# Optimization experiments

Measured on AMD Instinct MI355X. Metric: run time of the kernel, lower is better.

The kernel has to match this reference:

```python
import jax, jax.numpy as jnp
import numpy as np

B, N, M = 4, 512, 8192
QUERY_DIM, INPUT_DIM = 512, 256
HEADS, DIM_HEAD = 8, 64
ATT_DIM = HEADS * DIM_HEAD  # 512


def setup_inputs() -> dict:
    key = jax.random.key(0)
    ks = jax.random.split(key, 6)
    x = jax.random.normal(ks[0], (B, N, QUERY_DIM), dtype=jnp.float32)
    context = jax.random.normal(ks[1], (B, M, INPUT_DIM), dtype=jnp.float32)
    # Linear weights stored as [in, out] for x @ W
    Wq = jax.random.normal(ks[2], (QUERY_DIM, ATT_DIM), dtype=jnp.float32) / np.sqrt(QUERY_DIM)
    Wkv = jax.random.normal(ks[3], (INPUT_DIM, 2 * ATT_DIM), dtype=jnp.float32) / np.sqrt(INPUT_DIM)
    Wo = jax.random.normal(ks[4], (ATT_DIM, QUERY_DIM), dtype=jnp.float32) / np.sqrt(ATT_DIM)
    bo = jax.random.normal(ks[5], (QUERY_DIM,), dtype=jnp.float32) * 0.01
    return {"x": x, "context": context, "Wq": Wq, "Wkv": Wkv, "Wo": Wo, "bo": bo}


def reference(x, context, Wq, Wkv, Wo, bo):
    scale = DIM_HEAD ** -0.5
    q = x @ Wq                      # [B, N, H*D]
    kv = context @ Wkv              # [B, M, 2*H*D]
    k, v = jnp.split(kv, 2, axis=-1)
    # split heads: b n (h d) -> b h n d
    q = q.reshape(B, N, HEADS, DIM_HEAD).transpose(0, 2, 1, 3)
    k = k.reshape(B, M, HEADS, DIM_HEAD).transpose(0, 2, 1, 3)
    v = v.reshape(B, M, HEADS, DIM_HEAD).transpose(0, 2, 1, 3)
    scores = jnp.einsum('bhid,bhjd->bhij', q, k) * scale  # [B, H, N, M]
    attn = jax.nn.softmax(scores, axis=-1)
    out = jnp.einsum('bhij,bhjd->bhid', attn, v)           # [B, H, N, D]
    out = out.transpose(0, 2, 1, 3).reshape(B, N, ATT_DIM)
    return out @ Wo + bo
```

## Files before the change

kernel.cpp:

```cpp
#include <hip/hip_runtime.h>
#include <hip/hip_bf16.h>
#include <cstdint>

#define NB 4
#define NQ 512
#define NM 8192
#define NH 8
#define DH 64

typedef short bf16x8s __attribute__((ext_vector_type(8)));
typedef short bf16x4s __attribute__((ext_vector_type(4)));
typedef float f32x4  __attribute__((ext_vector_type(4)));

static __device__ __forceinline__ short f2bs(float f) {
    unsigned u = __builtin_bit_cast(unsigned, f);
    return (short)(unsigned short)((u + 0x8000u) >> 16);
}
static __device__ __forceinline__ unsigned pk2(float a, float b) {
    unsigned au = __builtin_bit_cast(unsigned, a) + 0x8000u;
    unsigned bu = __builtin_bit_cast(unsigned, b) + 0x8000u;
    return __builtin_amdgcn_perm(bu, au, 0x07060302u);
}

#if __has_builtin(__builtin_amdgcn_exp2f)
static __device__ __forceinline__ float fexp2(float x) { return __builtin_amdgcn_exp2f(x); }
#else
static __device__ __forceinline__ float fexp2(float x) { return exp2f(x); }
#endif

__global__ __launch_bounds__(256) void prep_weights(
    const float* __restrict__ Wq, const float* __restrict__ Wo,
    const float* __restrict__ Wkv,
    short* __restrict__ Wqf, short* __restrict__ Wof, short* __restrict__ Wkvf)
{
    const int t = threadIdx.x;
    const int w = t >> 6, ln = t & 63;
    const int m16 = ln & 15, quad = ln >> 4;
    int f = blockIdx.x * 4 + w;
    const float* src; short* dst; int N, KS, n0, ks;
    if (f < 512)       { src = Wq;  dst = Wqf;  N = 512;  KS = 16; n0 = f >> 4; ks = f & 15; }
    else if (f < 1024) { f -= 512;  src = Wo;  dst = Wof;  N = 512;  KS = 16; n0 = f >> 4; ks = f & 15; }
    else               { f -= 1024; src = Wkv; dst = Wkvf; N = 1024; KS = 8;  n0 = f >> 3; ks = f & 7; }
    const float* sp = src + (size_t)(ks * 32 + quad * 8) * N + n0 * 16 + m16;
    float v[8];
    #pragma unroll
    for (int j = 0; j < 8; ++j) v[j] = sp[(size_t)j * N];
    uint4 pkv = { pk2(v[0],v[1]), pk2(v[2],v[3]), pk2(v[4],v[5]), pk2(v[6],v[7]) };
    *(uint4*)(dst + ((size_t)(n0 * KS + ks) * 64 + ln) * 8) = pkv;
}

__device__ __forceinline__ void proj32_body(
    const float* __restrict__ A, const short* __restrict__ Wf,
    float* __restrict__ C, const float* __restrict__ bias,
    int tm, int tn, char* smemraw)
{
    short* As = (short*)smemraw;

    const int t = threadIdx.x;
    const int w = t >> 6, ln = t & 63;
    const int m16 = ln & 15, quad = ln >> 4;
    const int wm = w >> 1, wn = w & 1;

    const int ar = t >> 3, ac = (t & 7) << 3;

    const float* Ap = A + (size_t)(tm * 32 + ar) * 512 + ac;

    f32x4 acc[2] = {};

    {
        float4 a0 = *(const float4*)(Ap);
        float4 a1 = *(const float4*)(Ap + 4);
        uint4 wa = { pk2(a0.x,a0.y), pk2(a0.z,a0.w), pk2(a1.x,a1.y), pk2(a1.z,a1.w) };
        *(uint4*)&As[ar * 72 + ac] = wa;
    }

    #pragma unroll
    for (int k0 = 0; k0 < 512; k0 += 64) {
        short* Ab = As + ((k0 >> 6) & 1) * 2304;
        __syncthreads();

        bf16x8s bfr[2][2];
        #pragma unroll
        for (int ks = 0; ks < 2; ++ks)
            #pragma unroll
            for (int nt = 0; nt < 2; ++nt)
                bfr[ks][nt] = *(const bf16x8s*)(Wf +
                    ((size_t)((tn * 4 + wn * 2 + nt) * 16 + (k0 >> 5) + ks) * 64 + ln) * 8);

        bf16x8s afr[2];
        #pragma unroll
        for (int ks = 0; ks < 2; ++ks)
            afr[ks] = *(const bf16x8s*)&Ab[(wm * 16 + m16) * 72 + ks * 32 + quad * 8];

        float4 a0n, a1n;
        if (k0 + 64 < 512) {
            a0n = *(const float4*)(Ap + k0 + 64);
            a1n = *(const float4*)(Ap + k0 + 68);
        }

        #pragma unroll
        for (int ks = 0; ks < 2; ++ks)
            #pragma unroll
            for (int nt = 0; nt < 2; ++nt)
                acc[nt] = __builtin_amdgcn_mfma_f32_16x16x32_bf16(afr[ks], bfr[ks][nt], acc[nt], 0, 0, 0);

        if (k0 + 64 < 512) {
            short* Abn = As + ((((k0 >> 6) + 1) & 1)) * 2304;
            uint4 wa = { pk2(a0n.x,a0n.y), pk2(a0n.z,a0n.w), pk2(a1n.x,a1n.y), pk2(a1n.z,a1n.w) };
            *(uint4*)&Abn[ar * 72 + ac] = wa;
        }
    }

    const int row0 = tm * 32 + wm * 16 + quad * 4;
    const int col0 = tn * 64 + wn * 32;
    #pragma unroll
    for (int nt = 0; nt < 2; ++nt) {
        const int col = col0 + nt * 16 + m16;
        const float bb = bias ? bias[col] : 0.f;
        #pragma unroll
        for (int r = 0; r < 4; ++r)
            C[(size_t)(row0 + r) * 512 + col] = acc[nt][r] + bb;
    }
}

__device__ __forceinline__ void kv_body(
    const float* __restrict__ A, const short* __restrict__ Wkvf,
    short* __restrict__ Kf, short* __restrict__ Vf,
    int kvid, char* smemraw)
{
    short* As = (short*)smemraw;

    const int t  = threadIdx.x;
    const int tm = ((kvid >> 6) << 3) | (kvid & 7);
    const int tn = (kvid >> 3) & 7;
    const int w  = t >> 6, ln = t & 63;
    const int m16 = ln & 15, quad = ln >> 4;
    const int wm = w & 1, wn = w >> 1;

    const int ar = t >> 3;
    const int ac = (t & 7) << 2;

    const float* Abase = A + (size_t)(tm * 128 + ar) * 256 + ac;

    f32x4 acc[4][4] = {};

    {
        float4 av[4];
        #pragma unroll
        for (int p = 0; p < 4; ++p)
            av[p] = *(const float4*)(Abase + (size_t)p * 32 * 256);
        #pragma unroll
        for (int p = 0; p < 4; ++p) {
            uint2 wv = { pk2(av[p].x, av[p].y), pk2(av[p].z, av[p].w) };
            *(uint2*)&As[(p * 32 + ar) * 40 + ac] = wv;
        }
    }

    #pragma unroll
    for (int k0 = 0; k0 < 256; k0 += 32) {
        short* Ab = As + ((k0 >> 5) & 1) * 5120;
        __syncthreads();

        bf16x8s bfr[4];
        #pragma unroll
        for (int j = 0; j < 4; ++j)
            bfr[j] = *(const bf16x8s*)(Wkvf +
                ((size_t)((tn * 8 + wn * 4 + j) * 8 + (k0 >> 5)) * 64 + ln) * 8);

        bf16x8s af[4];
        #pragma unroll
        for (int i = 0; i < 4; ++i)
            af[i] = *(const bf16x8s*)&Ab[(wm * 64 + i * 16 + m16) * 40 + quad * 8];

        float4 avn[4];
        if (k0 + 32 < 256) {
            #pragma unroll
            for (int p = 0; p < 4; ++p)
                avn[p] = *(const float4*)(Abase + (size_t)p * 32 * 256 + k0 + 32);
        }

        #pragma unroll
        for (int i = 0; i < 4; ++i)
            #pragma unroll
            for (int j = 0; j < 4; ++j)
                acc[i][j] = __builtin_amdgcn_mfma_f32_16x16x32_bf16(af[i], bfr[j], acc[i][j], 0, 0, 0);

        if (k0 + 32 < 256) {
            short* Abn = As + (((k0 >> 5) + 1) & 1) * 5120;
            #pragma unroll
            for (int p = 0; p < 4; ++p) {
                uint2 wv = { pk2(avn[p].x, avn[p].y), pk2(avn[p].z, avn[p].w) };
                *(uint2*)&Abn[(p * 32 + ar) * 40 + ac] = wv;
            }
        }
    }

    const int col0 = tn * 128 + wn * 64;
    const int row0 = tm * 128 + wm * 64;
    const int b    = row0 >> 13;
    const int mr0  = row0 & (NM - 1);

    if (col0 < 512) {
        __syncthreads();
        const int h = col0 >> 6;
        short* Kp = Kf + (size_t)(b * NH + h) * (NM * DH);
        short* S  = (short*)smemraw + w * 2048;
        #pragma unroll
        for (int half = 0; half < 2; ++half) {
            const int i0 = half * 2;
            #pragma unroll
            for (int di = 0; di < 2; ++di)
                #pragma unroll
                for (int j = 0; j < 4; ++j) {
                    const int d    = j * 16 + m16;
                    const int fl   = di * 2 + (d >> 5);
                    const int base = fl * 512 + (((d >> 3) & 3) * 16 + quad * 4) * 8 + (d & 7);
                    #pragma unroll
                    for (int r = 0; r < 4; ++r)
                        S[base + r * 8] = f2bs(acc[i0 + di][j][r]);
                }
            const int gf0 = ((mr0 >> 4) + i0) * 2;
            #pragma unroll
            for (int fl = 0; fl < 4; ++fl) {
                uint4 v = *(const uint4*)&S[fl * 512 + ln * 8];
                *(uint4*)(Kp + ((size_t)(gf0 + fl) * 512 + ln * 8)) = v;
            }
        }
    } else {
        const int h = (col0 - 512) >> 6;
        short* Vp = Vf + (size_t)(b * NH + h) * (NM * DH);
        #pragma unroll
        for (int j = 0; j < 4; ++j)
            #pragma unroll
            for (int p = 0; p < 2; ++p) {
                uint4 v;
                v.x = pk2(acc[2*p    ][j][0], acc[2*p    ][j][1]);
                v.y = pk2(acc[2*p    ][j][2], acc[2*p    ][j][3]);
                v.z = pk2(acc[2*p + 1][j][0], acc[2*p + 1][j][1]);
                v.w = pk2(acc[2*p + 1][j][2], acc[2*p + 1][j][3]);
                *(uint4*)(Vp + ((size_t)(j * 256 + (mr0 >> 5) + p) * 64 + ln) * 8) = v;
            }
    }
}

__global__ __launch_bounds__(256) void gemm_kvq(
    const float* __restrict__ x,   const short* __restrict__ Wqf, float* __restrict__ q,
    const float* __restrict__ ctx, const short* __restrict__ Wkvf,
    short* __restrict__ Kf, short* __restrict__ Vf)
{
    __shared__ __align__(16) char smem[20480];
    if (blockIdx.x < 512)
        proj32_body(x, Wqf, q, nullptr, (int)(blockIdx.x >> 3), (int)(blockIdx.x & 7), smem);
    else
        kv_body(ctx, Wkvf, Kf, Vf, (int)(blockIdx.x - 512), smem);
}

__global__ __launch_bounds__(256) void gemm_proj32(
    const float* __restrict__ A, const short* __restrict__ Wf,
    float* __restrict__ C, const float* __restrict__ bias)
{
    __shared__ __align__(16) char smem[32 * 72 * 2 * 2];
    proj32_body(A, Wf, C, bias, (int)(blockIdx.x >> 3), (int)(blockIdx.x & 7), smem);
}

__global__ __launch_bounds__(512, 4) void attn_mfma(
    const float* __restrict__ Q,
    const short* __restrict__ Kfr,
    const short* __restrict__ Vfr,
    float* __restrict__ Og)
{
    __shared__ __align__(16) float Ob[2][32 * 66];
    __shared__ float lbuf[8 * 32];

    const int bid = blockIdx.x;
    const int xcd = bid & 7, g = bid >> 3;
    const int bh  = xcd * 4 + (g & 3);
    const int qt  = g >> 2;
    const int b   = bh >> 3, h = bh & 7;
    const int t   = threadIdx.x;
    const int w   = t >> 6, ln = t & 63;
    const int m16 = ln & 15, quad = ln >> 4;

    const short* Kbase = Kfr + (size_t)bh * (NM * DH);
    const short* Vbase = Vfr + (size_t)bh * (NM * DH);

    const float qsc = 0.125f * 1.44269504f;
    bf16x8s qf[2][2];
    #pragma unroll
    for (int mt = 0; mt < 2; ++mt) {
        const float* qrow = Q + ((size_t)(b * NQ + qt * 32 + mt * 16 + m16)) * 512 + h * 64;
        #pragma unroll
        for (int ks = 0; ks < 2; ++ks) {
            float4 x0 = *(const float4*)(qrow + ks * 32 + quad * 8);
            float4 x1 = *(const float4*)(qrow + ks * 32 + quad * 8 + 4);
            uint4 pkv = { pk2(x0.x * qsc, x0.y * qsc), pk2(x0.z * qsc, x0.w * qsc),
                          pk2(x1.x * qsc, x1.y * qsc), pk2(x1.z * qsc, x1.w * qsc) };
            qf[mt][ks] = *reinterpret_cast<bf16x8s*>(&pkv);
        }
    }

    bf16x4s ones4;
    #pragma unroll
    for (int j = 0; j < 4; ++j) ones4[j] = (short)0x3F80;

    f32x4 o[2][4] = {};
    f32x4 lsum[2] = {};

    bf16x8s kf[4][2];
    {
        const int kc = w * 64;
        #pragma unroll
        for (int nt = 0; nt < 4; ++nt)
            #pragma unroll
            for (int ks = 0; ks < 2; ++ks)
                kf[nt][ks] = *(const bf16x8s*)(Kbase + ((((kc >> 4) + nt) * 2 + ks) << 9) + ln * 8);
    }

    for (int it = 0; it < 16; ++it) {
        const int kc = it * 512 + w * 64;

        uint4 vraw[4][2];
        #pragma unroll
        for (int dt = 0; dt < 4; ++dt)
            #pragma unroll
            for (int kp = 0; kp < 2; ++kp)
                vraw[dt][kp] = *(const uint4*)(Vbase + ((size_t)(dt * 256 + (kc >> 5) + kp) * 64 + ln) * 8);

        f32x4 st[2][4] = {};
        #pragma unroll
        for (int kt = 0; kt < 4; ++kt)
            #pragma unroll
            for (int mt = 0; mt < 2; ++mt) {
                st[mt][kt] = __builtin_amdgcn_mfma_f32_16x16x32_bf16(kf[kt][0], qf[mt][0], st[mt][kt], 0, 0, 0);
                st[mt][kt] = __builtin_amdgcn_mfma_f32_16x16x32_bf16(kf[kt][1], qf[mt][1], st[mt][kt], 0, 0, 0);
            }

        if (it + 1 < 16) {
            const int kn = (it + 1) * 512 + w * 64;
            #pragma unroll
            for (int nt = 0; nt < 4; ++nt)
                #pragma unroll
                for (int ks = 0; ks < 2; ++ks)
                    kf[nt][ks] = *(const bf16x8s*)(Kbase + ((((kn >> 4) + nt) * 2 + ks) << 9) + ln * 8);
        }

        #pragma unroll
        for (int mt = 0; mt < 2; ++mt)
            #pragma unroll
            for (int kt = 0; kt < 4; ++kt) {
                const float p0 = fexp2(st[mt][kt][0]);
                const float p1 = fexp2(st[mt][kt][1]);
                const float p2 = fexp2(st[mt][kt][2]);
                const float p3 = fexp2(st[mt][kt][3]);
                uint2 pu = { pk2(p0, p1), pk2(p2, p3) };
                bf16x4s pbv = *reinterpret_cast<bf16x4s*>(&pu);
                const int kp = kt >> 1, hh = kt & 1;
                #pragma unroll
                for (int dt = 0; dt < 4; ++dt) {
                    uint2 vh = hh ? make_uint2(vraw[dt][kp].z, vraw[dt][kp].w)
                                  : make_uint2(vraw[dt][kp].x, vraw[dt][kp].y);
                    bf16x4s va = *reinterpret_cast<bf16x4s*>(&vh);
                    o[mt][dt] = __builtin_amdgcn_mfma_f32_16x16x16bf16_1k(va, pbv, o[mt][dt], 0, 0, 0);
                }
                lsum[mt] = __builtin_amdgcn_mfma_f32_16x16x16bf16_1k(ones4, pbv, lsum[mt], 0, 0, 0);
            }
    }

    if (quad == 0) {
        #pragma unroll
        for (int mt = 0; mt < 2; ++mt)
            lbuf[w * 32 + mt * 16 + m16] = lsum[mt][0];
    }
    if (w < 2) {
        float* dst = Ob[w];
        #pragma unroll
        for (int mt = 0; mt < 2; ++mt)
            #pragma unroll
            for (int dt = 0; dt < 4; ++dt)
                *(f32x4*)&dst[(mt * 16 + m16) * 66 + dt * 16 + quad * 4] = o[mt][dt];
    }
    __syncthreads();
    #pragma unroll
    for (int ph = 1; ph < 4; ++ph) {
        if ((w >> 1) == ph) {
            float* dst = Ob[w & 1];
            #pragma unroll
            for (int mt = 0; mt < 2; ++mt)
                #pragma unroll
                for (int dt = 0; dt < 4; ++dt) {
                    float* p = &dst[(mt * 16 + m16) * 66 + dt * 16 + quad * 4];
                    f32x4 cur = *(f32x4*)p;
                    cur += o[mt][dt];
                    *(f32x4*)p = cur;
                }
        }
        __syncthreads();
    }
    {
        const int row = t >> 4;
        const int d0  = (t & 15) << 2;
        float l = 0.f;
        #pragma unroll
        for (int wi = 0; wi < 8; ++wi) l += lbuf[wi * 32 + row];
        const float inv = 1.0f / l;
        float* op = Og + ((size_t)(b * NQ + qt * 32 + row)) * 512 + h * 64 + d0;
        const int c = row * 66 + d0;
        float4 r;
        r.x = (Ob[0][c + 0] + Ob[1][c + 0]) * inv;
        r.y = (Ob[0][c + 1] + Ob[1][c + 1]) * inv;
        r.z = (Ob[0][c + 2] + Ob[1][c + 2]) * inv;
        r.w = (Ob[0][c + 3] + Ob[1][c + 3]) * inv;
        *(float4*)op = r;
    }
}

extern "C" void kernel_launch(void* const* d_in, const int* in_sizes, int n_in,
                              void* d_out, int out_size, void* d_ws, size_t ws_size,
                              hipStream_t stream) {
    (void)in_sizes; (void)n_in; (void)out_size; (void)ws_size;

    const float* x   = (const float*)d_in[0];
    const float* ctx = (const float*)d_in[1];
    const float* Wq  = (const float*)d_in[2];
    const float* Wkv = (const float*)d_in[3];
    const float* Wo  = (const float*)d_in[4];
    const float* bo  = (const float*)d_in[5];
    float* out = (float*)d_out;

    float* ws    = (float*)d_ws;
    float* q     = ws;
    float* attno = q + (size_t)2048 * 512;
    short* Kf    = (short*)(attno + (size_t)2048 * 512);
    short* Vf    = Kf + (size_t)NB * NH * NM * DH;
    short* Wqf   = Vf + (size_t)NB * NH * NM * DH;
    short* Wof   = Wqf + (size_t)512 * 512;
    short* Wkvf  = Wof + (size_t)512 * 512;

    prep_weights<<<dim3(384), dim3(256), 0, stream>>>(Wq, Wo, Wkv, Wqf, Wof, Wkvf);

    gemm_kvq<<<dim3(2560), dim3(256), 0, stream>>>(x, Wqf, q, ctx, Wkvf, Kf, Vf);

    attn_mfma<<<dim3(512), dim3(512), 0, stream>>>(q, Kf, Vf, attno);

    gemm_proj32<<<dim3(512), dim3(256), 0, stream>>>(attno, Wof, out, bo);
}
```

Before: 188.9 us.

## Use 16x16x32 MFMA for PV and re-layout V tiles via LDS in kv projection

The attention PV product switches from pairs of 16x16x16 bf16 MFMAs to single 16x16x32 MFMAs, which halves the instruction count for the P·V and row-sum accumulation. To match the wider K operand, the V fragment layout written by the kv projection changes, so the kv epilogue now stages V through shared memory, like K already does, before writing it out. The K staging index math is also rewritten. The aim is higher matrix-core throughput in the dominant attention loop, at the cost of an extra LDS round trip and barrier in the projection epilogue.

```diff
diff --git a/kernel.cpp b/kernel.cpp
--- a/kernel.cpp
+++ b/kernel.cpp
@@ -52,11 +52,10 @@
 __device__ __forceinline__ void proj32_body(
     const float* __restrict__ A, const short* __restrict__ Wf,
     float* __restrict__ C, const float* __restrict__ bias,
-    int tm, int tn, char* smemraw)
+    int tm, int tn, char* smemraw, int t)
 {
     short* As = (short*)smemraw;
 
-    const int t = threadIdx.x;
     const int w = t >> 6, ln = t & 63;
     const int m16 = ln & 15, quad = ln >> 4;
     const int wm = w >> 1, wn = w & 1;
@@ -212,9 +211,10 @@
             for (int di = 0; di < 2; ++di)
                 #pragma unroll
                 for (int j = 0; j < 4; ++j) {
-                    const int d    = j * 16 + m16;
-                    const int fl   = di * 2 + (d >> 5);
-                    const int base = fl * 512 + (((d >> 3) & 3) * 16 + quad * 4) * 8 + (d & 7);
+                    const int base = ((quad & 1) * 2 + (j >> 1)) * 512
+                                   + (((j & 1) * 2 + (m16 >> 3)) * 16
+                                      + (di * 2 + (quad >> 1)) * 4) * 8
+                                   + (m16 & 7);
                     #pragma unroll
                     for (int r = 0; r < 4; ++r)
                         S[base + r * 8] = f2bs(acc[i0 + di][j][r]);
@@ -227,19 +227,30 @@
             }
         }
     } else {
+        __syncthreads();
         const int h = (col0 - 512) >> 6;
         short* Vp = Vf + (size_t)(b * NH + h) * (NM * DH);
-        #pragma unroll
-        for (int j = 0; j < 4; ++j)
-            #pragma unroll
-            for (int p = 0; p < 2; ++p) {
-                uint4 v;
-                v.x = pk2(acc[2*p    ][j][0], acc[2*p    ][j][1]);
-                v.y = pk2(acc[2*p    ][j][2], acc[2*p    ][j][3]);
-                v.z = pk2(acc[2*p + 1][j][0], acc[2*p + 1][j][1]);
-                v.w = pk2(acc[2*p + 1][j][2], acc[2*p + 1][j][3]);
-                *(uint4*)(Vp + ((size_t)(j * 256 + (mr0 >> 5) + p) * 64 + ln) * 8) = v;
+        short* S  = (short*)smemraw + w * 2048;
+        #pragma unroll
+        for (int half = 0; half < 2; ++half) {
+            const int i0 = half * 2;
+            #pragma unroll
+            for (int di = 0; di < 2; ++di)
+                #pragma unroll
+                for (int j = 0; j < 4; ++j) {
+                    const int base = j * 512 + (di * 2 + (quad >> 1)) * 128
+                                   + m16 * 8 + (quad & 1) * 4;
+                    #pragma unroll
+                    for (int r = 0; r < 4; ++r)
+                        S[base + r] = f2bs(acc[i0 + di][j][r]);
+                }
+            const int g0 = (mr0 >> 5) + half;
+            #pragma unroll
+            for (int fl = 0; fl < 4; ++fl) {
+                uint4 v = *(const uint4*)&S[fl * 512 + ln * 8];
+                *(uint4*)(Vp + ((size_t)(fl * 256 + g0) * 64 + ln) * 8) = v;
             }
+        }
     }
 }
 
@@ -250,7 +261,8 @@
 {
     __shared__ __align__(16) char smem[20480];
     if (blockIdx.x < 512)
-        proj32_body(x, Wqf, q, nullptr, (int)(blockIdx.x >> 3), (int)(blockIdx.x & 7), smem);
+        proj32_body(x, Wqf, q, nullptr, (int)(blockIdx.x >> 3), (int)(blockIdx.x & 7),
+                    smem, (int)threadIdx.x);
     else
         kv_body(ctx, Wkvf, Kf, Vf, (int)(blockIdx.x - 512), smem);
 }
@@ -260,7 +272,8 @@
     float* __restrict__ C, const float* __restrict__ bias)
 {
     __shared__ __align__(16) char smem[32 * 72 * 2 * 2];
-    proj32_body(A, Wf, C, bias, (int)(blockIdx.x >> 3), (int)(blockIdx.x & 7), smem);
+    proj32_body(A, Wf, C, bias, (int)(blockIdx.x >> 3), (int)(blockIdx.x & 7),
+                smem, (int)threadIdx.x);
 }
 
 __global__ __launch_bounds__(512, 4) void attn_mfma(
@@ -299,9 +312,9 @@
         }
     }
 
-    bf16x4s ones4;
-    #pragma unroll
-    for (int j = 0; j < 4; ++j) ones4[j] = (short)0x3F80;
+    bf16x8s ones8;
+    #pragma unroll
+    for (int j = 0; j < 8; ++j) ones8[j] = (short)0x3F80;
 
     f32x4 o[2][4] = {};
     f32x4 lsum[2] = {};
@@ -319,12 +332,12 @@
     for (int it = 0; it < 16; ++it) {
         const int kc = it * 512 + w * 64;
 
-        uint4 vraw[4][2];
+        bf16x8s va8[4][2];
         #pragma unroll
         for (int dt = 0; dt < 4; ++dt)
             #pragma unroll
-            for (int kp = 0; kp < 2; ++kp)
-                vraw[dt][kp] = *(const uint4*)(Vbase + ((size_t)(dt * 256 + (kc >> 5) + kp) * 64 + ln) * 8);
+            for (int gg = 0; gg < 2; ++gg)
+                va8[dt][gg] = *(const bf16x8s*)(Vbase + ((size_t)(dt * 256 + (kc >> 5) + gg) * 64 + ln) * 8);
 
         f32x4 st[2][4] = {};
         #pragma unroll
@@ -347,22 +360,16 @@
         #pragma unroll
         for (int mt = 0; mt < 2; ++mt)
             #pragma unroll
-            for (int kt = 0; kt < 4; ++kt) {
-                const float p0 = fexp2(st[mt][kt][0]);
-                const float p1 = fexp2(st[mt][kt][1]);
-                const float p2 = fexp2(st[mt][kt][2]);
-                const float p3 = fexp2(st[mt][kt][3]);
-                uint2 pu = { pk2(p0, p1), pk2(p2, p3) };
-                bf16x4s pbv = *reinterpret_cast<bf16x4s*>(&pu);
-                const int kp = kt >> 1, hh = kt & 1;
+            for (int gg = 0; gg < 2; ++gg) {
+                const f32x4 s0 = st[mt][2 * gg];
+                const f32x4 s1 = st[mt][2 * gg + 1];
+                uint4 pu = { pk2(fexp2(s0[0]), fexp2(s0[1])), pk2(fexp2(s0[2]), fexp2(s0[3])),
+                             pk2(fexp2(s1[0]), fexp2(s1[1])), pk2(fexp2(s1[2]), fexp2(s1[3])) };
+                bf16x8s pbv = *reinterpret_cast<bf16x8s*>(&pu);
                 #pragma unroll
-                for (int dt = 0; dt < 4; ++dt) {
-                    uint2 vh = hh ? make_uint2(vraw[dt][kp].z, vraw[dt][kp].w)
-                                  : make_uint2(vraw[dt][kp].x, vraw[dt][kp].y);
-                    bf16x4s va = *reinterpret_cast<bf16x4s*>(&vh);
-                    o[mt][dt] = __builtin_amdgcn_mfma_f32_16x16x16bf16_1k(va, pbv, o[mt][dt], 0, 0, 0);
-                }
-                lsum[mt] = __builtin_amdgcn_mfma_f32_16x16x16bf16_1k(ones4, pbv, lsum[mt], 0, 0, 0);
+                for (int dt = 0; dt < 4; ++dt)
+                    o[mt][dt] = __builtin_amdgcn_mfma_f32_16x16x32_bf16(va8[dt][gg], pbv, o[mt][dt], 0, 0, 0);
+                lsum[mt] = __builtin_amdgcn_mfma_f32_16x16x32_bf16(ones8, pbv, lsum[mt], 0, 0, 0);
             }
     }
 
```

Result: no change. 185.4 us (-1.9%).
